# Kernel optimization log

Measured on AMD Instinct MI355X. Metric: run time of the kernel, lower is better.

## Reference

```python
import jax, jax.numpy as jnp
import numpy as np

N, E, D, O, STEP = 100000, 640000, 128, 64, 10


def setup_inputs() -> dict:
    key = jax.random.key(0)
    k1, k2, k3, k4, k5 = jax.random.split(key, 5)
    x = jax.random.normal(k1, (N, D), dtype=jnp.float32)
    edge_index = jax.random.randint(k2, (2, E), 0, N, dtype=jnp.int64)
    t = jax.random.normal(k3, (STEP, D), dtype=jnp.float32)
    W = jax.random.normal(k4, (O, D), dtype=jnp.float32) * 0.05
    b = jax.random.normal(k5, (O,), dtype=jnp.float32) * 0.05
    return {"x": x, "edge_index": edge_index, "t": t, "W": W, "b": b}


def reference(x, edge_index, t, W, b):
    n = x.shape[0]
    # add self loops
    loops = jnp.arange(n, dtype=edge_index.dtype)
    row = jnp.concatenate([edge_index[0], loops])  # source (x_j)
    col = jnp.concatenate([edge_index[1], loops])  # target (aggregation index)
    # symmetric normalization: deg computed over col (targets)
    deg = jax.ops.segment_sum(jnp.ones_like(row, dtype=x.dtype), col, num_segments=n)
    dinv = deg ** -0.5  # deg >= 1 thanks to self loops
    norm = (dinv[row] * dinv[col])[:, None]  # [E+N, 1]
    # per-channel softmax over the 10 hop weights
    t_norm = jax.nn.softmax(t, axis=0)  # [STEP, D]

    def hop(carry, tk):
        h, y = carry
        h = jax.ops.segment_sum(norm * h[row], col, num_segments=n)  # SpMM hop
        return (h, y + tk * h), None

    (_, y), _ = jax.lax.scan(hop, (x, t_norm[0] * x), t_norm[1:])
    return y @ W.T + b
```

## Files before the change

### kernel.cpp

```cpp
#include <hip/hip_runtime.h>

typedef _Float16 half2_t __attribute__((ext_vector_type(2)));
typedef unsigned int uint;

#define D 128
#define O 64

static inline size_t align_up(size_t x, size_t a) { return (x + a - 1) & ~(a - 1); }


__global__ void init_deg_k(int* __restrict__ deg, int n) {
  int i = blockIdx.x * blockDim.x + threadIdx.x;
  if (i < n) deg[i] = 1;
}

__global__ void count_deg_k(const int* __restrict__ col, int* __restrict__ deg, int E, int n) {
  int i = blockIdx.x * blockDim.x + threadIdx.x;
  if (i >= E) return;
  int c = col[i];
  if ((unsigned)c >= (unsigned)n) return;
  atomicAdd(&deg[c], 1);
}

__global__ void dinv_k(const int* __restrict__ deg, float* __restrict__ dinv, int n) {
  int i = blockIdx.x * blockDim.x + threadIdx.x;
  if (i < n) dinv[i] = rsqrtf((float)deg[i]);
}

__global__ void scan1_k(const int* __restrict__ deg, int* __restrict__ row_ptr,
                        int* __restrict__ bsum, int n) {
  __shared__ int s[256];
  int tid = threadIdx.x;
  int gid = blockIdx.x * 256 + tid;
  int v = (gid < n) ? (deg[gid] - 1) : 0;
  s[tid] = v;
  __syncthreads();
  for (int off = 1; off < 256; off <<= 1) {
    int t = (tid >= off) ? s[tid - off] : 0;
    __syncthreads();
    s[tid] += t;
    __syncthreads();
  }
  if (gid < n) row_ptr[gid] = s[tid] - v;
  if (tid == 255) bsum[blockIdx.x] = s[255];
}

__global__ void scan2_k(int* __restrict__ bsum, int nb) {
  __shared__ int s[512];
  int tid = threadIdx.x;
  int v = (tid < nb) ? bsum[tid] : 0;
  s[tid] = v;
  __syncthreads();
  for (int off = 1; off < 512; off <<= 1) {
    int t = (tid >= off) ? s[tid - off] : 0;
    __syncthreads();
    s[tid] += t;
    __syncthreads();
  }
  if (tid < nb) bsum[tid] = s[tid] - v;
}

__global__ void scan3_k(const int* __restrict__ bsum, const int* __restrict__ deg,
                        int* __restrict__ row_ptr, int* __restrict__ cursor, int n) {
  int gid = blockIdx.x * 256 + threadIdx.x;
  if (gid < n) {
    int r = row_ptr[gid] + bsum[blockIdx.x];
    row_ptr[gid] = r;
    cursor[gid] = r;
    if (gid == n - 1) row_ptr[n] = r + deg[gid] - 1;
  }
}

__global__ void fill_k(const int* __restrict__ rows, const int* __restrict__ cols,
                       int* __restrict__ cursor, const float* __restrict__ dinv,
                       int* __restrict__ csr_src, float* __restrict__ csr_norm, int E, int n) {
  int i = blockIdx.x * blockDim.x + threadIdx.x;
  if (i >= E) return;
  int u = rows[i], v = cols[i];
  if ((unsigned)v >= (unsigned)n) return;
  if ((unsigned)u >= (unsigned)n) u = 0;
  int slot = atomicAdd(&cursor[v], 1);
  csr_src[slot] = u;
  csr_norm[slot] = dinv[u] * dinv[v];
}

__global__ void softmax_k(const float* __restrict__ t, float* __restrict__ tn, int step) {
  int d = threadIdx.x;
  if (d >= D) return;
  float vals[16];
  float m = -1e30f;
  for (int k = 0; k < step; ++k) { vals[k] = t[k * D + d]; m = fmaxf(m, vals[k]); }
  float ssum = 0.f;
  for (int k = 0; k < step; ++k) { vals[k] = expf(vals[k] - m); ssum += vals[k]; }
  float inv = 1.f / ssum;
  for (int k = 0; k < step; ++k) tn[k * D + d] = vals[k] * inv;
}

__global__ void pack_w_k(const float* __restrict__ W, uint* __restrict__ Wpk, int total) {
  int i = blockIdx.x * blockDim.x + threadIdx.x;
  if (i >= total) return;
  int o = i >> 6, dd = i & 63;
  half2_t h;
  h.x = (_Float16)W[o * D + 2 * dd];
  h.y = (_Float16)W[o * D + 2 * dd + 1];
  Wpk[i] = *(uint*)&h;
}

__global__ void init_h_k(const float* __restrict__ x, half2_t* __restrict__ h0, int total) {
  int i = blockIdx.x * blockDim.x + threadIdx.x;
  if (i >= total) return;
  float2 v = ((const float2*)x)[i];
  half2_t o;
  o.x = (_Float16)v.x;
  o.y = (_Float16)v.y;
  h0[i] = o;
}

#define UNR 8
template <int DO_Y>
__global__ __launch_bounds__(256) void hop_k(
    const half2_t* __restrict__ h_old, half2_t* __restrict__ h_new, half2_t* __restrict__ y,
    const int* __restrict__ row_ptr, const int* __restrict__ csr_src,
    const float* __restrict__ csr_norm, const float* __restrict__ dinv,
    const float* __restrict__ tprev, const float* __restrict__ tcur, int n) {
  int wid = (blockIdx.x * blockDim.x + threadIdx.x) >> 6;
  int lane = threadIdx.x & 63;
  if (wid >= n) return;
  int v = __builtin_amdgcn_readfirstlane(wid);
  float dv = dinv[v];
  float ns = dv * dv;
  half2_t hv = h_old[(size_t)v * 64 + lane];
  float hx = (float)hv.x, hy = (float)hv.y;
  float ax = ns * hx, ay = ns * hy;
  int beg = __builtin_amdgcn_readfirstlane(row_ptr[v]);
  int end = __builtin_amdgcn_readfirstlane(row_ptr[v + 1]);
  for (int i = beg; i < end; i += UNR) {
    int u[UNR];
    float w[UNR];
#pragma unroll
    for (int j = 0; j < UNR; ++j) {
      int ic = i + j;
      int icl = (ic < end - 1) ? ic : (end - 1);
      u[j] = csr_src[icl];
      float wj = csr_norm[icl];
      w[j] = (ic < end) ? wj : 0.f;
    }
    half2_t g[UNR];
#pragma unroll
    for (int j = 0; j < UNR; ++j) g[j] = h_old[(size_t)u[j] * 64 + lane];
#pragma unroll
    for (int j = 0; j < UNR; ++j) {
      ax += w[j] * (float)g[j].x;
      ay += w[j] * (float)g[j].y;
    }
  }
  half2_t hn;
  hn.x = (_Float16)ax;
  hn.y = (_Float16)ay;
  h_new[(size_t)v * 64 + lane] = hn;
  if (DO_Y) {
    float2 ta = ((const float2*)tprev)[lane];
    float2 tb = ((const float2*)tcur)[lane];
    float yx = ta.x * hx + tb.x * ax;
    float yy = ta.y * hy + tb.y * ay;
    if (DO_Y == 2) {
      half2_t yo = y[(size_t)v * 64 + lane];
      yx += (float)yo.x;
      yy += (float)yo.y;
    }
    half2_t yn;
    yn.x = (_Float16)yx;
    yn.y = (_Float16)yy;
    y[(size_t)v * 64 + lane] = yn;
  }
}


__global__ __launch_bounds__(256) void proj_k(
    const uint* __restrict__ y, const uint* __restrict__ Wpk,
    const float* __restrict__ b, float* __restrict__ out, int n, int nwaves) {
  int lane = threadIdx.x & 63;
  int wid = (blockIdx.x * blockDim.x + threadIdx.x) >> 6;
  uint wreg[64];
  const uint* wp = Wpk + lane * 64;
#pragma unroll
  for (int j = 0; j < 64; ++j) wreg[j] = wp[j];
  float bias = b[lane];
  for (int v = wid; v < n; v += nwaves) {
    int vu = __builtin_amdgcn_readfirstlane(v);
    const uint* yrow = y + (size_t)vu * 64;
    float acc = bias;
#pragma unroll
    for (int dd = 0; dd < 64; ++dd) {
      uint yv = yrow[dd];
#if defined(__has_builtin) && __has_builtin(__builtin_amdgcn_fdot2)
      acc = __builtin_amdgcn_fdot2(*(half2_t*)&yv, *(half2_t*)&wreg[dd], acc, false);
#else
      half2_t yh = *(half2_t*)&yv, wh = *(half2_t*)&wreg[dd];
      acc += (float)yh.x * (float)wh.x + (float)yh.y * (float)wh.y;
#endif
    }
    out[(size_t)vu * O + lane] = acc;
  }
}


extern "C" void kernel_launch(void* const* d_in, const int* in_sizes, int n_in,
                              void* d_out, int out_size, void* d_ws, size_t ws_size,
                              hipStream_t stream) {
  const float* x = (const float*)d_in[0];
  const int* ei = (const int*)d_in[1];
  const float* t = (const float*)d_in[2];
  const float* W = (const float*)d_in[3];
  const float* b = (const float*)d_in[4];
  float* out = (float*)d_out;

  int n = in_sizes[0] / D;
  int E = in_sizes[1] / 2;
  int step = in_sizes[2] / D;
  const int* rows = ei;
  const int* cols = ei + E;

  char* p = (char*)d_ws;
  auto alloc = [&](size_t bytes) { char* r = p; p += align_up(bytes, 256); return r; };
  int*     deg      = (int*)alloc((size_t)n * 4);
  float*   dinv     = (float*)alloc((size_t)n * 4);
  int*     row_ptr  = (int*)alloc((size_t)(n + 1) * 4);
  int*     cursor   = (int*)alloc((size_t)n * 4);
  int*     bsum     = (int*)alloc(2048);
  int*     csr_src  = (int*)alloc((size_t)E * 4);
  float*   csr_norm = (float*)alloc((size_t)E * 4);
  float*   tn       = (float*)alloc((size_t)step * D * 4);
  uint*    Wpk      = (uint*)alloc((size_t)O * 64 * 4);
  half2_t* h_a      = (half2_t*)alloc((size_t)n * 64 * 4);
  half2_t* h_b      = (half2_t*)alloc((size_t)n * 64 * 4);
  half2_t* y        = (half2_t*)alloc((size_t)n * 64 * 4);

  int nb1 = (n + 255) / 256;
  init_deg_k<<<nb1, 256, 0, stream>>>(deg, n);
  count_deg_k<<<(E + 255) / 256, 256, 0, stream>>>(cols, deg, E, n);
  dinv_k<<<nb1, 256, 0, stream>>>(deg, dinv, n);
  scan1_k<<<nb1, 256, 0, stream>>>(deg, row_ptr, bsum, n);
  scan2_k<<<1, 512, 0, stream>>>(bsum, nb1);
  scan3_k<<<nb1, 256, 0, stream>>>(bsum, deg, row_ptr, cursor, n);
  fill_k<<<(E + 255) / 256, 256, 0, stream>>>(rows, cols, cursor, dinv, csr_src, csr_norm, E, n);
  softmax_k<<<1, 128, 0, stream>>>(t, tn, step);
  pack_w_k<<<(O * 64 + 255) / 256, 256, 0, stream>>>(W, Wpk, O * 64);
  init_h_k<<<((size_t)n * 64 + 255) / 256, 256, 0, stream>>>(x, h_a, n * 64);

  half2_t* ho = h_a;
  half2_t* hn = h_b;
  int hop_blocks = (n + 3) / 4;
  for (int k = 1; k < step; ++k) {
    const float* tp = tn + (size_t)(k - 1) * D;
    const float* tc = tn + (size_t)k * D;
    if (k & 1) {
      if (k == 1)
        hop_k<1><<<hop_blocks, 256, 0, stream>>>(ho, hn, y, row_ptr, csr_src, csr_norm, dinv, tp, tc, n);
      else
        hop_k<2><<<hop_blocks, 256, 0, stream>>>(ho, hn, y, row_ptr, csr_src, csr_norm, dinv, tp, tc, n);
    } else {
      hop_k<0><<<hop_blocks, 256, 0, stream>>>(ho, hn, y, row_ptr, csr_src, csr_norm, dinv, tp, tc, n);
    }
    half2_t* tmp = ho; ho = hn; hn = tmp;
  }

  int proj_blocks = 512;
  int nwaves = proj_blocks * 4;
  proj_k<<<proj_blocks, 256, 0, stream>>>((const uint*)y, Wpk, b, out, n, nwaves);
}
```

Baseline: 586.4 us.

## Process four nodes per wave in hop kernel and fold dinv into scan

Each wave in the hop kernel now handles four destination nodes. It issues the first eight neighbor gathers for all four nodes together, which raises memory-level parallelism and amortises per-wave setup, then finishes any leftover edges node by node. The separate dinv kernel is merged into scan1 to save one launch and one read of the degree array. The cost is higher register pressure from the 4x8 arrays and four times fewer waves launched. Nodes with low degree also waste masked gather slots.

```diff
diff --git a/kernel.cpp b/kernel.cpp
--- a/kernel.cpp
+++ b/kernel.cpp
@@ -22,17 +22,14 @@
   atomicAdd(&deg[c], 1);
 }
 
-__global__ void dinv_k(const int* __restrict__ deg, float* __restrict__ dinv, int n) {
-  int i = blockIdx.x * blockDim.x + threadIdx.x;
-  if (i < n) dinv[i] = rsqrtf((float)deg[i]);
-}
-
 __global__ void scan1_k(const int* __restrict__ deg, int* __restrict__ row_ptr,
-                        int* __restrict__ bsum, int n) {
+                        int* __restrict__ bsum, float* __restrict__ dinv, int n) {
   __shared__ int s[256];
   int tid = threadIdx.x;
   int gid = blockIdx.x * 256 + tid;
-  int v = (gid < n) ? (deg[gid] - 1) : 0;
+  int dg = (gid < n) ? deg[gid] : 1;
+  if (gid < n) dinv[gid] = rsqrtf((float)dg);
+  int v = (gid < n) ? (dg - 1) : 0;
   s[tid] = v;
   __syncthreads();
   for (int off = 1; off < 256; off <<= 1) {
@@ -117,61 +114,113 @@
 }
 
 #define UNR 8
+#define NPW 4
 template <int DO_Y>
 __global__ __launch_bounds__(256) void hop_k(
     const half2_t* __restrict__ h_old, half2_t* __restrict__ h_new, half2_t* __restrict__ y,
     const int* __restrict__ row_ptr, const int* __restrict__ csr_src,
     const float* __restrict__ csr_norm, const float* __restrict__ dinv,
     const float* __restrict__ tprev, const float* __restrict__ tcur, int n) {
-  int wid = (blockIdx.x * blockDim.x + threadIdx.x) >> 6;
+  int wave = (blockIdx.x * blockDim.x + threadIdx.x) >> 6;
   int lane = threadIdx.x & 63;
-  if (wid >= n) return;
-  int v = __builtin_amdgcn_readfirstlane(wid);
-  float dv = dinv[v];
-  float ns = dv * dv;
-  half2_t hv = h_old[(size_t)v * 64 + lane];
-  float hx = (float)hv.x, hy = (float)hv.y;
-  float ax = ns * hx, ay = ns * hy;
-  int beg = __builtin_amdgcn_readfirstlane(row_ptr[v]);
-  int end = __builtin_amdgcn_readfirstlane(row_ptr[v + 1]);
-  for (int i = beg; i < end; i += UNR) {
-    int u[UNR];
-    float w[UNR];
+  int v0 = wave * NPW;
+  if (v0 >= n) return;
+  v0 = __builtin_amdgcn_readfirstlane(v0);
+
+  int beg[NPW], end[NPW];
+  float ax[NPW], ay[NPW], hx[NPW], hy[NPW];
+#pragma unroll
+  for (int m = 0; m < NPW; ++m) {
+    int vm = v0 + m;
+    if (vm > n - 1) vm = n - 1;
+    beg[m] = __builtin_amdgcn_readfirstlane(row_ptr[vm]);
+    end[m] = __builtin_amdgcn_readfirstlane(row_ptr[vm + 1]);
+    float dv = dinv[vm];
+    float ns = dv * dv;
+    half2_t hv = h_old[(size_t)vm * 64 + lane];
+    hx[m] = (float)hv.x;
+    hy[m] = (float)hv.y;
+    ax[m] = ns * hx[m];
+    ay[m] = ns * hy[m];
+  }
+
+  int uu[NPW][UNR];
+  float ww[NPW][UNR];
+#pragma unroll
+  for (int m = 0; m < NPW; ++m) {
 #pragma unroll
     for (int j = 0; j < UNR; ++j) {
-      int ic = i + j;
-      int icl = (ic < end - 1) ? ic : (end - 1);
-      u[j] = csr_src[icl];
+      int ic = beg[m] + j;
+      int icl = ic < end[m] - 1 ? ic : end[m] - 1;
+      if (icl < 0) icl = 0;
+      uu[m][j] = csr_src[icl];
       float wj = csr_norm[icl];
-      w[j] = (ic < end) ? wj : 0.f;
-    }
-    half2_t g[UNR];
-#pragma unroll
-    for (int j = 0; j < UNR; ++j) g[j] = h_old[(size_t)u[j] * 64 + lane];
+      ww[m][j] = (ic < end[m]) ? wj : 0.f;
+    }
+  }
+  half2_t g[NPW][UNR];
+#pragma unroll
+  for (int m = 0; m < NPW; ++m)
+#pragma unroll
+    for (int j = 0; j < UNR; ++j) g[m][j] = h_old[(size_t)uu[m][j] * 64 + lane];
+#pragma unroll
+  for (int m = 0; m < NPW; ++m)
 #pragma unroll
     for (int j = 0; j < UNR; ++j) {
-      ax += w[j] * (float)g[j].x;
-      ay += w[j] * (float)g[j].y;
-    }
-  }
-  half2_t hn;
-  hn.x = (_Float16)ax;
-  hn.y = (_Float16)ay;
-  h_new[(size_t)v * 64 + lane] = hn;
+      ax[m] += ww[m][j] * (float)g[m][j].x;
+      ay[m] += ww[m][j] * (float)g[m][j].y;
+    }
+
+#pragma unroll
+  for (int m = 0; m < NPW; ++m) {
+    for (int i = beg[m] + UNR; i < end[m]; i += UNR) {
+      int u2[UNR];
+      float w2[UNR];
+#pragma unroll
+      for (int j = 0; j < UNR; ++j) {
+        int ic = i + j;
+        int icl = ic < end[m] - 1 ? ic : end[m] - 1;
+        u2[j] = csr_src[icl];
+        float wj = csr_norm[icl];
+        w2[j] = (ic < end[m]) ? wj : 0.f;
+      }
+      half2_t g2[UNR];
+#pragma unroll
+      for (int j = 0; j < UNR; ++j) g2[j] = h_old[(size_t)u2[j] * 64 + lane];
+#pragma unroll
+      for (int j = 0; j < UNR; ++j) {
+        ax[m] += w2[j] * (float)g2[j].x;
+        ay[m] += w2[j] * (float)g2[j].y;
+      }
+    }
+  }
+
+  float2 ta, tb;
   if (DO_Y) {
-    float2 ta = ((const float2*)tprev)[lane];
-    float2 tb = ((const float2*)tcur)[lane];
-    float yx = ta.x * hx + tb.x * ax;
-    float yy = ta.y * hy + tb.y * ay;
-    if (DO_Y == 2) {
-      half2_t yo = y[(size_t)v * 64 + lane];
-      yx += (float)yo.x;
-      yy += (float)yo.y;
-    }
-    half2_t yn;
-    yn.x = (_Float16)yx;
-    yn.y = (_Float16)yy;
-    y[(size_t)v * 64 + lane] = yn;
+    ta = ((const float2*)tprev)[lane];
+    tb = ((const float2*)tcur)[lane];
+  }
+#pragma unroll
+  for (int m = 0; m < NPW; ++m) {
+    int vm = v0 + m;
+    if (vm >= n) break;
+    half2_t hn;
+    hn.x = (_Float16)ax[m];
+    hn.y = (_Float16)ay[m];
+    h_new[(size_t)vm * 64 + lane] = hn;
+    if (DO_Y) {
+      float yx = ta.x * hx[m] + tb.x * ax[m];
+      float yy = ta.y * hy[m] + tb.y * ay[m];
+      if (DO_Y == 2) {
+        half2_t yo = y[(size_t)vm * 64 + lane];
+        yx += (float)yo.x;
+        yy += (float)yo.y;
+      }
+      half2_t yn;
+      yn.x = (_Float16)yx;
+      yn.y = (_Float16)yy;
+      y[(size_t)vm * 64 + lane] = yn;
+    }
   }
 }
 
@@ -239,8 +288,7 @@
   int nb1 = (n + 255) / 256;
   init_deg_k<<<nb1, 256, 0, stream>>>(deg, n);
   count_deg_k<<<(E + 255) / 256, 256, 0, stream>>>(cols, deg, E, n);
-  dinv_k<<<nb1, 256, 0, stream>>>(deg, dinv, n);
-  scan1_k<<<nb1, 256, 0, stream>>>(deg, row_ptr, bsum, n);
+  scan1_k<<<nb1, 256, 0, stream>>>(deg, row_ptr, bsum, dinv, n);
   scan2_k<<<1, 512, 0, stream>>>(bsum, nb1);
   scan3_k<<<nb1, 256, 0, stream>>>(bsum, deg, row_ptr, cursor, n);
   fill_k<<<(E + 255) / 256, 256, 0, stream>>>(rows, cols, cursor, dinv, csr_src, csr_norm, E, n);
@@ -250,7 +298,7 @@
 
   half2_t* ho = h_a;
   half2_t* hn = h_b;
-  int hop_blocks = (n + 3) / 4;
+  int hop_blocks = (n + NPW * 4 - 1) / (NPW * 4);
   for (int k = 1; k < step; ++k) {
     const float* tp = tn + (size_t)(k - 1) * D;
     const float* tc = tn + (size_t)k * D;
```

After: 608.2 us. 3.7% more time.
